# Optimization experiments

Hardware: AMD Instinct MI355X
Metric: run time of the kernel (lower is better)

Reference implementation:

```python
import jax, jax.numpy as jnp
import numpy as np

D_MODEL = 1024
N_HEADS = 16
D_K = D_MODEL // N_HEADS

def _xavier(key, shape):
    fan_in, fan_out = shape[1], shape[0]
    limit = float(np.sqrt(6.0 / (fan_in + fan_out)))
    return jax.random.uniform(key, shape, jnp.float32, -limit, limit)

def setup_inputs() -> dict:
    key = jax.random.key(0)
    ks = jax.random.split(key, 7)
    B, S = 2, 2048
    return {
        "query": jax.random.normal(ks[0], (B, S, D_MODEL), jnp.float32),
        "key": jax.random.normal(ks[1], (B, S, D_MODEL), jnp.float32),
        "value": jax.random.normal(ks[2], (B, S, D_MODEL), jnp.float32),
        "w_q": _xavier(ks[3], (D_MODEL, D_MODEL)),  # torch Linear weight [out, in]
        "w_k": _xavier(ks[4], (D_MODEL, D_MODEL)),
        "w_v": _xavier(ks[5], (D_MODEL, D_MODEL)),
        "w_o": _xavier(ks[6], (D_MODEL, D_MODEL)),
        "ln_gamma": jnp.ones((D_MODEL,), jnp.float32),
        "ln_beta": jnp.zeros((D_MODEL,), jnp.float32),
    }

def reference(query, key, value, w_q, w_k, w_v, w_o, ln_gamma, ln_beta):
    B, S, _ = query.shape
    # projections (torch Linear: x @ W.T), split into heads -> [B, H, S, d_k]
    def split_heads(x, W):
        return (x @ W.T).reshape(B, S, N_HEADS, D_K).transpose(0, 2, 1, 3)
    Q = split_heads(query, w_q)
    K = split_heads(key, w_k)
    V = split_heads(value, w_v)
    scores = jnp.einsum('bhqd,bhkd->bhqk', Q, K) / jnp.sqrt(jnp.float32(D_K))
    attn = jax.nn.softmax(scores, axis=-1)  # dropout disabled (p=0 / eval)
    ctx = jnp.einsum('bhqk,bhkd->bhqd', attn, V)
    ctx = ctx.transpose(0, 2, 1, 3).reshape(B, S, D_MODEL)
    out = ctx @ w_o.T
    # residual + LayerNorm
    x = query + out
    mu = jnp.mean(x, axis=-1, keepdims=True)
    var = jnp.var(x, axis=-1, keepdims=True)
    return (x - mu) / jnp.sqrt(var + 1e-5) * ln_gamma + ln_beta
```

## Files before the change

### kernel.cpp

```cpp
#include <hip/hip_runtime.h>
#include <hip/hip_bf16.h>

#define DEVI __device__ __forceinline__

typedef float f32x4 __attribute__((ext_vector_type(4)));
typedef short bf16x8 __attribute__((ext_vector_type(8)));
typedef unsigned short ushort_t;

DEVI ushort_t f2bf(float x) {
  union { float f; unsigned u; } c; c.f = x;
  unsigned u = c.u;
  unsigned r = (u + 0x7fffu + ((u >> 16) & 1u)) >> 16;
  return (ushort_t)r;
}

DEVI float bf2f(unsigned hw) {
  union { unsigned u; float f; } c; c.u = hw << 16; return c.f;
}

DEVI unsigned cvt_pk_bf16(float lo, float hi) {
  unsigned r;
  asm volatile("v_cvt_pk_bf16_f32 %0, %1, %2" : "=v"(r) : "v"(lo), "v"(hi));
  return r;
}

DEVI void gload16(const ushort_t* g, ushort_t* l) {
  __builtin_amdgcn_global_load_lds(
      (const __attribute__((address_space(1))) unsigned int*)g,
      (__attribute__((address_space(3))) unsigned int*)l, 16, 0, 0);
}


__global__ __launch_bounds__(256)
void cvt_w_kernel(const float* __restrict__ w0, const float* __restrict__ w1,
                  const float* __restrict__ w2, const float* __restrict__ w3,
                  ushort_t* __restrict__ q0, ushort_t* __restrict__ q1,
                  ushort_t* __restrict__ q2, ushort_t* __restrict__ q3) {
  int z = blockIdx.y;
  int i = blockIdx.x * 256 + threadIdx.x;
  const float* in = (z == 0) ? w0 : (z == 1) ? w1 : (z == 2) ? w2 : w3;
  ushort_t* out = (z == 0) ? q0 : (z == 1) ? q1 : (z == 2) ? q2 : q3;
  const float4* p = (const float4*)in + (size_t)i * 2;
  float4 a = p[0], b = p[1];
  uint4 v;
  v.x = cvt_pk_bf16(a.x, a.y);
  v.y = cvt_pk_bf16(a.z, a.w);
  v.z = cvt_pk_bf16(b.x, b.y);
  v.w = cvt_pk_bf16(b.z, b.w);
  ((uint4*)out)[i] = v;
}


__global__ __launch_bounds__(256)
void gemm128(const void* A0v, const void* A1v, const void* A2v,
             const void* W0v, const void* W1v, const void* W2v,
             void* __restrict__ O0, void* __restrict__ O1,
             void* __restrict__ O2, int mode_base, int nsteps, float qscale) {
  constexpr int K = 1024;
  int z = blockIdx.z;
  int mode = (mode_base == 3) ? 3 : mode_base + z;
  const void* Av = (z == 0) ? A0v : (z == 1) ? A1v : A2v;
  const void* Wv = (z == 0) ? W0v : (z == 1) ? W1v : W2v;
  void* Op = (z == 0) ? O0 : (z == 1) ? O1 : O2;
  if (mode == 3) {
    Av = (const ushort_t*)A0v + z * 512;
    Wv = (const ushort_t*)W0v + z * 512;
    Op = z ? O1 : O0;
  }
  bool aF32 = (mode <= 1);
  bool bF32 = (mode == 2);
  bool fused = aF32 || bF32;
  float scale = (mode == 0) ? qscale : 1.0f;
  int m0 = (mode == 2) ? blockIdx.y * 128 : blockIdx.x * 128;
  int n0 = (mode == 2) ? blockIdx.x * 128 : blockIdx.y * 128;

  __shared__ __align__(16) ushort_t Asm[128 * 64];
  __shared__ __align__(16) ushort_t Bsm[128 * 64];

  int t = threadIdx.x;
  int lane = t & 63, wave = t >> 6;
  int wm = wave >> 1, wn = wave & 1;
  int col = lane & 15, g = lane >> 4;
  int lr = lane >> 3, lc = lane & 7;
  int cswz = col & 7;

  int rowA = m0 + wave * 32 + lr;
  int rowB = n0 + wave * 32 + lr;
  const ushort_t* aSrcB = (const ushort_t*)Av + (size_t)rowA * K + (lc ^ lr) * 8;
  const ushort_t* bSrcB = (const ushort_t*)Wv + (size_t)rowB * K + (lc ^ lr) * 8;
  const float* fSrc = aF32
      ? ((const float*)Av + (size_t)rowA * K + (lc ^ lr) * 8)
      : ((const float*)Wv + (size_t)rowB * K + (lc ^ lr) * 8);
  ushort_t* fDst = aF32 ? Asm : Bsm;
  int fOffBase = (wave * 32 + lr) * 64 + lc * 8;

  f32x4 z4 = {0.f, 0.f, 0.f, 0.f};
  f32x4 acc[4][4];
  for (int i = 0; i < 4; i++)
    for (int j = 0; j < 4; j++) acc[i][j] = z4;

  float4 fr[4][2];

#define FLOAD(koff) do {                                                   \
    _Pragma("unroll")                                                      \
    for (int i_ = 0; i_ < 4; i_++) {                                       \
      const float* p_ = fSrc + (size_t)(i_ * 8) * K + (koff);              \
      fr[i_][0] = *(const float4*)p_;                                      \
      fr[i_][1] = *(const float4*)(p_ + 4);                                \
    }                                                                      \
  } while (0)

#define FWRITE() do {                                                      \
    _Pragma("unroll")                                                      \
    for (int i_ = 0; i_ < 4; i_++) {                                       \
      uint4 w_;                                                            \
      w_.x = cvt_pk_bf16(fr[i_][0].x, fr[i_][0].y);                        \
      w_.y = cvt_pk_bf16(fr[i_][0].z, fr[i_][0].w);                        \
      w_.z = cvt_pk_bf16(fr[i_][1].x, fr[i_][1].y);                        \
      w_.w = cvt_pk_bf16(fr[i_][1].z, fr[i_][1].w);                        \
      *(uint4*)(fDst + fOffBase + i_ * 8 * 64) = w_;                       \
    }                                                                      \
  } while (0)

  if (fused) FLOAD(0);

  for (int kt = 0; kt < nsteps; ++kt) {
    int koff = kt * 64;
    if (fused) FWRITE();
    if (!aF32) {
#pragma unroll
      for (int i_ = 0; i_ < 4; i_++)
        gload16(aSrcB + koff + i_ * 8 * K, &Asm[(wave * 32 + i_ * 8) * 64]);
    }
    if (!bF32) {
#pragma unroll
      for (int i_ = 0; i_ < 4; i_++)
        gload16(bSrcB + koff + i_ * 8 * K, &Bsm[(wave * 32 + i_ * 8) * 64]);
    }
    __syncthreads();
    if (fused && kt + 1 < nsteps) FLOAD(koff + 64);
#pragma unroll
    for (int kk = 0; kk < 2; ++kk) {
      bf16x8 af[4], bfr[4];
#pragma unroll
      for (int mi = 0; mi < 4; mi++) {
        int row = wm * 64 + mi * 16 + col;
        af[mi] = *(const bf16x8*)(Asm + row * 64 + (((kk * 4 + g) ^ cswz) * 8));
      }
#pragma unroll
      for (int ni = 0; ni < 4; ni++) {
        int row = wn * 64 + ni * 16 + col;
        bfr[ni] = *(const bf16x8*)(Bsm + row * 64 + (((kk * 4 + g) ^ cswz) * 8));
      }
      __builtin_amdgcn_s_setprio(1);
#pragma unroll
      for (int mi = 0; mi < 4; mi++)
#pragma unroll
        for (int ni = 0; ni < 4; ni++)
          acc[mi][ni] = __builtin_amdgcn_mfma_f32_16x16x32_bf16(af[mi], bfr[ni],
                                                                acc[mi][ni], 0, 0, 0);
      __builtin_amdgcn_s_setprio(0);
    }
    __syncthreads();
  }

#pragma unroll
  for (int mi = 0; mi < 4; mi++)
#pragma unroll
    for (int ni = 0; ni < 4; ni++)
#pragma unroll
      for (int r = 0; r < 4; r++) {
        int m = m0 + wm * 64 + mi * 16 + g * 4 + r;
        int n = n0 + wn * 64 + ni * 16 + col;
        float v = acc[mi][ni][r] * scale;
        if (mode <= 1) {
          int b = m >> 11, s = m & 2047, h = n >> 6, d = n & 63;
          ((ushort_t*)Op)[(((size_t)(b * 16 + h) * 2048 + s) * 64) + d] = f2bf(v);
        } else if (mode == 2) {
          int h = m >> 6, d = m & 63, b = n >> 11, s = n & 2047;
          ((ushort_t*)Op)[(((size_t)(b * 16 + h) * 64 + d) * 2048) + s] = f2bf(v);
        } else {
          ((ushort_t*)Op)[(size_t)m * 1024 + n] = f2bf(v);
        }
      }
#undef FLOAD
#undef FWRITE
}


__global__ __launch_bounds__(256, 3)
void attn_kernel(const ushort_t* __restrict__ Qh, const ushort_t* __restrict__ Kh,
                 const ushort_t* __restrict__ Vt,
                 ushort_t* __restrict__ op0, ushort_t* __restrict__ op1,
                 float* __restrict__ lp0, float* __restrict__ lp1) {
  int bh = blockIdx.x;
  int qt = blockIdx.y;
  int sp = blockIdx.z;
  int t = threadIdx.x, lane = t & 63, wave = t >> 6;
  int col = lane & 15, g = lane >> 4;
  int lr = lane >> 3, lc = lane & 7;
  int cswz = col & 7;
  int q0 = qt * 128 + wave * 32;
  int kbase = sp * 1024;
  ushort_t* opart = sp ? op1 : op0;
  float* lpart = sp ? lp1 : lp0;

  const ushort_t* Qp = Qh + (size_t)bh * 2048 * 64;
  const ushort_t* Kp = Kh + (size_t)bh * 2048 * 64;
  const ushort_t* Vp = Vt + (size_t)bh * 64 * 2048;

  __shared__ __align__(16) ushort_t Ksm[2][64 * 64];
  __shared__ __align__(16) ushort_t Vsm[2][64 * 64];

  int slot0 = wave * 16 + lr;
  int slot1 = slot0 + 8;
  int key0 = (slot0 & 0x20) | ((slot0 & 0x0C) << 1) | ((slot0 & 0x10) >> 2) | (slot0 & 3);
  int key1 = (slot1 & 0x20) | ((slot1 & 0x0C) << 1) | ((slot1 & 0x10) >> 2) | (slot1 & 3);

  const ushort_t* kSrc0 = Kp + (size_t)key0 * 64 + (lc ^ lr) * 8;
  const ushort_t* kSrc1 = Kp + (size_t)key1 * 64 + (lc ^ lr) * 8;
  const ushort_t* vSrc = Vp + (size_t)(wave * 16 + lr) * 2048 + (lc ^ lr) * 8;

#define ATTN_STAGE(buf, k0) do { \
    gload16(kSrc0 + (size_t)(k0) * 64, &Ksm[buf][wave * 1024]);        \
    gload16(kSrc1 + (size_t)(k0) * 64, &Ksm[buf][wave * 1024 + 512]);  \
    gload16(vSrc + (k0),               &Vsm[buf][wave * 1024]);        \
    gload16(vSrc + (k0) + 16384,       &Vsm[buf][wave * 1024 + 512]);  \
  } while (0)

  bf16x8 qa0 = *(const bf16x8*)(Qp + (size_t)(q0 + col) * 64 + g * 8);
  bf16x8 qa1 = *(const bf16x8*)(Qp + (size_t)(q0 + col) * 64 + 32 + g * 8);
  bf16x8 qb0 = *(const bf16x8*)(Qp + (size_t)(q0 + 16 + col) * 64 + g * 8);
  bf16x8 qb1 = *(const bf16x8*)(Qp + (size_t)(q0 + 16 + col) * 64 + 32 + g * 8);

  f32x4 z4 = {0.f, 0.f, 0.f, 0.f};
  f32x4 oa[4], ob[4];
  for (int i = 0; i < 4; i++) { oa[i] = z4; ob[i] = z4; }
  f32x4 la = z4, lb = z4;

  ATTN_STAGE(0, kbase);
  __syncthreads();

  for (int it = 0; it < 16; ++it) {
    int cur = it & 1;
    int k0 = kbase + it * 64;
    if (it < 15) ATTN_STAGE(cur ^ 1, k0 + 64);

    const ushort_t* Ks = Ksm[cur];
    const ushort_t* Vs = Vsm[cur];

    f32x4 sa[4], sb[4];
#pragma unroll
    for (int kt = 0; kt < 4; kt++) {
      int off = (kt * 16 + col) * 64 + ((g ^ cswz) * 8);
      bf16x8 kf0 = *(const bf16x8*)(Ks + off);
      bf16x8 kf1 = *(const bf16x8*)(Ks + (off ^ 32));
      f32x4 a = z4, b = z4;
      __builtin_amdgcn_s_setprio(1);
      a = __builtin_amdgcn_mfma_f32_16x16x32_bf16(kf0, qa0, a, 0, 0, 0);
      a = __builtin_amdgcn_mfma_f32_16x16x32_bf16(kf1, qa1, a, 0, 0, 0);
      b = __builtin_amdgcn_mfma_f32_16x16x32_bf16(kf0, qb0, b, 0, 0, 0);
      b = __builtin_amdgcn_mfma_f32_16x16x32_bf16(kf1, qb1, b, 0, 0, 0);
      __builtin_amdgcn_s_setprio(0);
      sa[kt] = a; sb[kt] = b;
    }

    unsigned pka[8], pkb[8];
#pragma unroll
    for (int kt = 0; kt < 4; kt++) {
      float a0 = __builtin_amdgcn_exp2f(sa[kt][0]);
      float a1 = __builtin_amdgcn_exp2f(sa[kt][1]);
      float a2 = __builtin_amdgcn_exp2f(sa[kt][2]);
      float a3 = __builtin_amdgcn_exp2f(sa[kt][3]);
      la[0] += a0; la[1] += a1; la[2] += a2; la[3] += a3;
      pka[2 * kt]     = cvt_pk_bf16(a0, a1);
      pka[2 * kt + 1] = cvt_pk_bf16(a2, a3);
      float b0 = __builtin_amdgcn_exp2f(sb[kt][0]);
      float b1 = __builtin_amdgcn_exp2f(sb[kt][1]);
      float b2 = __builtin_amdgcn_exp2f(sb[kt][2]);
      float b3 = __builtin_amdgcn_exp2f(sb[kt][3]);
      lb[0] += b0; lb[1] += b1; lb[2] += b2; lb[3] += b3;
      pkb[2 * kt]     = cvt_pk_bf16(b0, b1);
      pkb[2 * kt + 1] = cvt_pk_bf16(b2, b3);
    }

#pragma unroll
    for (int kk = 0; kk < 2; kk++) {
      union { uint4 u; bf16x8 f; } ua, ub;
      ua.u.x = pka[4 * kk];     ua.u.y = pka[4 * kk + 1];
      ua.u.z = pka[4 * kk + 2]; ua.u.w = pka[4 * kk + 3];
      ub.u.x = pkb[4 * kk];     ub.u.y = pkb[4 * kk + 1];
      ub.u.z = pkb[4 * kk + 2]; ub.u.w = pkb[4 * kk + 3];
      __builtin_amdgcn_s_setprio(1);
#pragma unroll
      for (int dt = 0; dt < 4; dt++) {
        bf16x8 vf = *(const bf16x8*)(Vs + (dt * 16 + col) * 64 +
                                     (((kk * 4 + g) ^ cswz) * 8));
        oa[dt] = __builtin_amdgcn_mfma_f32_16x16x32_bf16(vf, ua.f, oa[dt], 0, 0, 0);
        ob[dt] = __builtin_amdgcn_mfma_f32_16x16x32_bf16(vf, ub.f, ob[dt], 0, 0, 0);
      }
      __builtin_amdgcn_s_setprio(0);
    }
    __syncthreads();
  }
#undef ATTN_STAGE

  float lva = (la[0] + la[1]) + (la[2] + la[3]);
  lva += __shfl_xor(lva, 16);
  lva += __shfl_xor(lva, 32);
  float lvb = (lb[0] + lb[1]) + (lb[2] + lb[3]);
  lvb += __shfl_xor(lvb, 16);
  lvb += __shfl_xor(lvb, 32);
  if (g == 0) {
    lpart[(size_t)bh * 2048 + q0 + col] = lva;
    lpart[(size_t)bh * 2048 + q0 + 16 + col] = lvb;
  }
  int b = bh >> 4, h = bh & 15;
#pragma unroll
  for (int dt = 0; dt < 4; dt++)
#pragma unroll
    for (int rp = 0; rp < 2; rp++) {
      int d = dt * 16 + g * 4 + rp * 2;
      unsigned pa = cvt_pk_bf16(oa[dt][rp * 2], oa[dt][rp * 2 + 1]);
      unsigned pb = cvt_pk_bf16(ob[dt][rp * 2], ob[dt][rp * 2 + 1]);
      *(unsigned*)(opart + ((size_t)(b * 2048 + q0 + col)) * 1024 + h * 64 + d) = pa;
      *(unsigned*)(opart + ((size_t)(b * 2048 + q0 + 16 + col)) * 1024 + h * 64 + d) = pb;
    }
}


__global__ __launch_bounds__(256)
void attn_reduce(const ushort_t* __restrict__ o0, const ushort_t* __restrict__ o1,
                 const float* __restrict__ l0, const float* __restrict__ l1,
                 ushort_t* __restrict__ ctx) {
  int m = blockIdx.x;
  int t = threadIdx.x;
  int b = m >> 11, q = m & 2047;
  int h = t >> 4;
  size_t li = (size_t)(b * 16 + h) * 2048 + q;
  float inv = 1.0f / (l0[li] + l1[li]);
  uint2 a = ((const uint2*)(o0 + (size_t)m * 1024))[t];
  uint2 c = ((const uint2*)(o1 + (size_t)m * 1024))[t];
  float x0 = (bf2f(a.x & 0xffffu) + bf2f(c.x & 0xffffu)) * inv;
  float x1 = (bf2f(a.x >> 16)     + bf2f(c.x >> 16))     * inv;
  float x2 = (bf2f(a.y & 0xffffu) + bf2f(c.y & 0xffffu)) * inv;
  float x3 = (bf2f(a.y >> 16)     + bf2f(c.y >> 16))     * inv;
  uint2 o;
  o.x = cvt_pk_bf16(x0, x1);
  o.y = cvt_pk_bf16(x2, x3);
  ((uint2*)(ctx + (size_t)m * 1024))[t] = o;
}


__global__ __launch_bounds__(256)
void ln_kernel(const float* __restrict__ resid, const ushort_t* __restrict__ p0,
               const ushort_t* __restrict__ p1,
               const float* __restrict__ gamma, const float* __restrict__ beta,
               float* __restrict__ out) {
  int m = blockIdx.x;
  int t = threadIdx.x;
  int lane = t & 63, wave = t >> 6;
  float4 a = ((const float4*)(resid + (size_t)m * 1024))[t];
  uint2 v0 = ((const uint2*)(p0 + (size_t)m * 1024))[t];
  uint2 v1 = ((const uint2*)(p1 + (size_t)m * 1024))[t];
  float4 x;
  x.x = a.x + bf2f(v0.x & 0xffffu) + bf2f(v1.x & 0xffffu);
  x.y = a.y + bf2f(v0.x >> 16)     + bf2f(v1.x >> 16);
  x.z = a.z + bf2f(v0.y & 0xffffu) + bf2f(v1.y & 0xffffu);
  x.w = a.w + bf2f(v0.y >> 16)     + bf2f(v1.y >> 16);
  float sum = (x.x + x.y) + (x.z + x.w);
  float ssq = x.x * x.x + x.y * x.y + x.z * x.z + x.w * x.w;
  for (int off = 1; off < 64; off <<= 1) {
    sum += __shfl_xor(sum, off);
    ssq += __shfl_xor(ssq, off);
  }
  __shared__ float red[8];
  if (lane == 0) { red[wave] = sum; red[4 + wave] = ssq; }
  __syncthreads();
  sum = red[0] + red[1] + red[2] + red[3];
  ssq = red[4] + red[5] + red[6] + red[7];
  float mu = sum * (1.f / 1024.f);
  float var = ssq * (1.f / 1024.f) - mu * mu;
  float rstd = rsqrtf(var + 1e-5f);
  const float4* gp = (const float4*)gamma;
  const float4* bp = (const float4*)beta;
  float4 gg = gp[t], bb = bp[t];
  float4 y;
  y.x = (x.x - mu) * rstd * gg.x + bb.x;
  y.y = (x.y - mu) * rstd * gg.y + bb.y;
  y.z = (x.z - mu) * rstd * gg.z + bb.z;
  y.w = (x.w - mu) * rstd * gg.w + bb.w;
  ((float4*)(out + (size_t)m * 1024))[t] = y;
}


extern "C" void kernel_launch(void* const* d_in, const int* in_sizes, int n_in,
                              void* d_out, int out_size, void* d_ws, size_t ws_size,
                              hipStream_t stream) {
  (void)in_sizes; (void)n_in; (void)out_size; (void)ws_size;
  const float* query = (const float*)d_in[0];
  const float* keyi  = (const float*)d_in[1];
  const float* value = (const float*)d_in[2];
  const float* w_q = (const float*)d_in[3];
  const float* w_k = (const float*)d_in[4];
  const float* w_v = (const float*)d_in[5];
  const float* w_o = (const float*)d_in[6];
  const float* ln_g = (const float*)d_in[7];
  const float* ln_b = (const float*)d_in[8];

  char* ws = (char*)d_ws;
  const size_t MB = 1u << 20;
  ushort_t* op0 = (ushort_t*)(ws + 0 * MB);
  ushort_t* op1 = (ushort_t*)(ws + 8 * MB);
  float*    l0  = (float*)   (ws + 16 * MB);
  float*    l1  = (float*)   (ws + 17 * MB);
  ushort_t* proj0 = (ushort_t*)(ws + 0 * MB);
  ushort_t* proj1 = (ushort_t*)(ws + 8 * MB);
  ushort_t* Wq  = (ushort_t*)(ws + 24 * MB);
  ushort_t* Wk  = (ushort_t*)(ws + 26 * MB);
  ushort_t* Wv  = (ushort_t*)(ws + 28 * MB);
  ushort_t* Wo  = (ushort_t*)(ws + 30 * MB);
  ushort_t* Qh  = (ushort_t*)(ws + 32 * MB);
  ushort_t* Kh  = (ushort_t*)(ws + 40 * MB);
  ushort_t* Vt  = (ushort_t*)(ws + 48 * MB);
  ushort_t* ctx = (ushort_t*)(ws + 56 * MB);

  const float SCL = 0.18033688f;

  cvt_w_kernel<<<dim3(512, 4), 256, 0, stream>>>(w_q, w_k, w_v, w_o,
                                                 Wq, Wk, Wv, Wo);

  gemm128<<<dim3(32, 8, 3), 256, 0, stream>>>(query, keyi, Wv,
                                              Wq, Wk, value,
                                              Qh, Kh, Vt, 0, 16, SCL);
  attn_kernel<<<dim3(32, 16, 2), 256, 0, stream>>>(Qh, Kh, Vt,
                                                   op0, op1, l0, l1);
  attn_reduce<<<4096, 256, 0, stream>>>(op0, op1, l0, l1, ctx);
  gemm128<<<dim3(32, 8, 2), 256, 0, stream>>>(ctx, ctx, ctx, Wo, Wo, Wo,
                                              proj0, proj1, proj0, 3, 8, 1.0f);
  ln_kernel<<<4096, 256, 0, stream>>>(query, proj0, proj1, ln_g, ln_b,
                                      (float*)d_out);
}
```

Baseline: 123.9 us.

## Double-buffer GEMM shared-memory tiles to overlap loads with MFMA compute

Turns the A and B shared-memory tiles of the projection GEMM into two buffers. The next K-step's tile, including the fp32-to-bf16 converted tile, is written into the alternate buffer while MFMAs run on the current one, and the loop drops to one barrier per iteration. This is meant to hide global-load and LDS-write latency behind compute. In exchange, LDS use doubles to 64KB per block, which may reduce occupancy.

```diff
diff --git a/kernel.cpp b/kernel.cpp
--- a/kernel.cpp
+++ b/kernel.cpp
@@ -74,8 +74,8 @@
   int m0 = (mode == 2) ? blockIdx.y * 128 : blockIdx.x * 128;
   int n0 = (mode == 2) ? blockIdx.x * 128 : blockIdx.y * 128;
 
-  __shared__ __align__(16) ushort_t Asm[128 * 64];
-  __shared__ __align__(16) ushort_t Bsm[128 * 64];
+  __shared__ __align__(16) ushort_t Asm[2][128 * 64];
+  __shared__ __align__(16) ushort_t Bsm[2][128 * 64];
 
   int t = threadIdx.x;
   int lane = t & 63, wave = t >> 6;
@@ -91,7 +91,6 @@
   const float* fSrc = aF32
       ? ((const float*)Av + (size_t)rowA * K + (lc ^ lr) * 8)
       : ((const float*)Wv + (size_t)rowB * K + (lc ^ lr) * 8);
-  ushort_t* fDst = aF32 ? Asm : Bsm;
   int fOffBase = (wave * 32 + lr) * 64 + lc * 8;
 
   f32x4 z4 = {0.f, 0.f, 0.f, 0.f};
@@ -110,7 +109,8 @@
     }                                                                      \
   } while (0)
 
-#define FWRITE() do {                                                      \
+#define FWRITE(buf) do {                                                   \
+    ushort_t* fd_ = aF32 ? &Asm[buf][0] : &Bsm[buf][0];                    \
     _Pragma("unroll")                                                      \
     for (int i_ = 0; i_ < 4; i_++) {                                       \
       uint4 w_;                                                            \
@@ -118,39 +118,51 @@
       w_.y = cvt_pk_bf16(fr[i_][0].z, fr[i_][0].w);                        \
       w_.z = cvt_pk_bf16(fr[i_][1].x, fr[i_][1].y);                        \
       w_.w = cvt_pk_bf16(fr[i_][1].z, fr[i_][1].w);                        \
-      *(uint4*)(fDst + fOffBase + i_ * 8 * 64) = w_;                       \
+      *(uint4*)(fd_ + fOffBase + i_ * 8 * 64) = w_;                        \
     }                                                                      \
   } while (0)
 
-  if (fused) FLOAD(0);
+#define GLOADS(buf, koff) do {                                             \
+    if (!aF32) {                                                           \
+      _Pragma("unroll")                                                    \
+      for (int i_ = 0; i_ < 4; i_++)                                       \
+        gload16(aSrcB + (koff) + i_ * 8 * K,                               \
+                &Asm[buf][(wave * 32 + i_ * 8) * 64]);                     \
+    }                                                                      \
+    if (!bF32) {                                                           \
+      _Pragma("unroll")                                                    \
+      for (int i_ = 0; i_ < 4; i_++)                                       \
+        gload16(bSrcB + (koff) + i_ * 8 * K,                               \
+                &Bsm[buf][(wave * 32 + i_ * 8) * 64]);                     \
+    }                                                                      \
+  } while (0)
+
+  if (fused) { FLOAD(0); FWRITE(0); }
+  GLOADS(0, 0);
+  if (fused && nsteps > 1) FLOAD(64);
+  __syncthreads();
 
   for (int kt = 0; kt < nsteps; ++kt) {
-    int koff = kt * 64;
-    if (fused) FWRITE();
-    if (!aF32) {
-#pragma unroll
-      for (int i_ = 0; i_ < 4; i_++)
-        gload16(aSrcB + koff + i_ * 8 * K, &Asm[(wave * 32 + i_ * 8) * 64]);
-    }
-    if (!bF32) {
-#pragma unroll
-      for (int i_ = 0; i_ < 4; i_++)
-        gload16(bSrcB + koff + i_ * 8 * K, &Bsm[(wave * 32 + i_ * 8) * 64]);
-    }
-    __syncthreads();
-    if (fused && kt + 1 < nsteps) FLOAD(koff + 64);
+    int cur = kt & 1;
+    if (kt + 1 < nsteps) {
+      if (fused) FWRITE(cur ^ 1);
+      GLOADS(cur ^ 1, (kt + 1) * 64);
+      if (fused && kt + 2 < nsteps) FLOAD((kt + 2) * 64);
+    }
 #pragma unroll
     for (int kk = 0; kk < 2; ++kk) {
       bf16x8 af[4], bfr[4];
 #pragma unroll
       for (int mi = 0; mi < 4; mi++) {
         int row = wm * 64 + mi * 16 + col;
-        af[mi] = *(const bf16x8*)(Asm + row * 64 + (((kk * 4 + g) ^ cswz) * 8));
+        af[mi] = *(const bf16x8*)(&Asm[cur][0] + row * 64 +
+                                  (((kk * 4 + g) ^ cswz) * 8));
       }
 #pragma unroll
       for (int ni = 0; ni < 4; ni++) {
         int row = wn * 64 + ni * 16 + col;
-        bfr[ni] = *(const bf16x8*)(Bsm + row * 64 + (((kk * 4 + g) ^ cswz) * 8));
+        bfr[ni] = *(const bf16x8*)(&Bsm[cur][0] + row * 64 +
+                                   (((kk * 4 + g) ^ cswz) * 8));
       }
       __builtin_amdgcn_s_setprio(1);
 #pragma unroll
@@ -185,6 +197,7 @@
       }
 #undef FLOAD
 #undef FWRITE
+#undef GLOADS
 }
 
 
```

New measurement: 128.9 us. 4.0% more time.
